# Performance work log

Hardware: AMD Instinct MI355X
Metric: run time of the kernel (lower is better)

The kernel has to match this reference:

```python
import jax, jax.numpy as jnp
import numpy as np

B, C, V, L = 64, 32, 1024, 12
ORDER = 2


def setup_inputs() -> dict:
    key = jax.random.key(0)
    ks = jax.random.split(key, 6)
    x = jax.random.normal(ks[0], (B, C, V, L), dtype=jnp.float32)
    A1 = jax.random.uniform(ks[1], (V, V), dtype=jnp.float32)
    A2 = jax.random.uniform(ks[2], (V, V), dtype=jnp.float32)
    nodevec1 = jax.random.normal(ks[3], (V, 10), dtype=jnp.float32)
    nodevec2 = jax.random.normal(ks[4], (10, V), dtype=jnp.float32)
    c_cat = (ORDER * 3 + 1) * C  # 7*C = 224, matches gcn: (order*support_len+1)*c_in
    W_mlp = jax.random.normal(ks[5], (C, c_cat), dtype=jnp.float32) * 0.05
    b_mlp = jnp.zeros((C,), dtype=jnp.float32)
    return {"x": x, "A1": A1, "A2": A2, "nodevec1": nodevec1,
            "nodevec2": nodevec2, "W_mlp": W_mlp, "b_mlp": b_mlp}


def reference(x, A1, A2, nodevec1, nodevec2, W_mlp, b_mlp):
    # adaptive adjacency: softmax(relu(E1 @ E2), dim=1)  (graph-wavenet style)
    adp = jax.nn.softmax(jax.nn.relu(nodevec1 @ nodevec2), axis=1)  # [V, V]
    supports = (A1, A2, adp)
    # gcn.forward: multi-hop diffusion via nconv einsum, order=2
    out = [x]
    for a in supports:
        x1 = jnp.einsum('ncvl,vw->ncwl', x, a)   # hop 1
        out.append(x1)
        x2 = jnp.einsum('ncvl,vw->ncwl', x1, a)  # hop 2
        out.append(x2)
    h = jnp.concatenate(out, axis=1)             # [B, 7C, V, L]
    # linear: 1x1 Conv2d over channel dim (dropout is identity in eval)
    h = jnp.einsum('ncvl,oc->novl', h, W_mlp) + b_mlp[None, :, None, None]
    return h
```

## Files before the change

### kernel.cpp

```cpp
#include <hip/hip_runtime.h>
#include <hip/hip_bf16.h>


typedef __attribute__((ext_vector_type(8))) short short8;
typedef __attribute__((ext_vector_type(4))) float floatx4;

#define V_DIM 1024
#define L_DIM 12
#define B_DIM 64
#define C_DIM 32

__global__ __launch_bounds__(128) void adp_kernel(
    const float* __restrict__ nv1, const float* __restrict__ nv2,
    float* __restrict__ adp) {
  const int v = blockIdx.x, tid = threadIdx.x;
  float n1[10];
#pragma unroll
  for (int i = 0; i < 10; ++i) n1[i] = nv1[v * 10 + i];
  __shared__ float red[128];
  float e[8];
  float lmax = -1e30f;
#pragma unroll
  for (int j = 0; j < 8; ++j) {
    int w = tid + j * 128;
    float s = 0.f;
#pragma unroll
    for (int i = 0; i < 10; ++i) s += n1[i] * nv2[i * V_DIM + w];
    s = fmaxf(s, 0.f);
    e[j] = s;
    lmax = fmaxf(lmax, s);
  }
  red[tid] = lmax; __syncthreads();
  for (int s = 64; s > 0; s >>= 1) {
    if (tid < s) red[tid] = fmaxf(red[tid], red[tid + s]);
    __syncthreads();
  }
  float mx = red[0]; __syncthreads();
  float lsum = 0.f;
#pragma unroll
  for (int j = 0; j < 8; ++j) { e[j] = __expf(e[j] - mx); lsum += e[j]; }
  red[tid] = lsum; __syncthreads();
  for (int s = 64; s > 0; s >>= 1) {
    if (tid < s) red[tid] += red[tid + s];
    __syncthreads();
  }
  float inv = 1.f / red[0];
#pragma unroll
  for (int j = 0; j < 8; ++j) adp[(size_t)v * V_DIM + tid + j * 128] = e[j] * inv;
}

__global__ __launch_bounds__(256) void cast_transpose(
    const float* __restrict__ A1, const float* __restrict__ A2,
    const float* __restrict__ adp, __hip_bfloat16* __restrict__ As,
    __hip_bfloat16* __restrict__ BtCat) {
  const int z = blockIdx.z;
  const float* src = (z == 0) ? A1 : (z == 1) ? A2 : adp;
  __hip_bfloat16* sdst = As + (size_t)z * V_DIM * V_DIM;
  __hip_bfloat16* tdst = BtCat + (size_t)(2 * z) * V_DIM * V_DIM;
  __shared__ float tile[64][65];
  const int v0 = blockIdx.y * 64, w0 = blockIdx.x * 64;
  const int tc = threadIdx.x & 15, tr = threadIdx.x >> 4;
#pragma unroll
  for (int i = 0; i < 4; ++i) {
    int r = tr + i * 16;
    float4 val = *(const float4*)(src + (size_t)(v0 + r) * V_DIM + w0 + tc * 4);
    tile[r][tc * 4 + 0] = val.x; tile[r][tc * 4 + 1] = val.y;
    tile[r][tc * 4 + 2] = val.z; tile[r][tc * 4 + 3] = val.w;
    __hip_bfloat16* sp = sdst + (size_t)(v0 + r) * V_DIM + w0 + tc * 4;
    sp[0] = __float2bfloat16(val.x); sp[1] = __float2bfloat16(val.y);
    sp[2] = __float2bfloat16(val.z); sp[3] = __float2bfloat16(val.w);
  }
  __syncthreads();
#pragma unroll
  for (int i = 0; i < 4; ++i) {
    int r = tr + i * 16;
    __hip_bfloat16* tp = tdst + (size_t)(w0 + r) * V_DIM + v0 + tc * 4;
#pragma unroll
    for (int j = 0; j < 4; ++j) tp[j] = __float2bfloat16(tile[tc * 4 + j][r]);
  }
}

__global__ __launch_bounds__(256) void transpose_x_k(
    const float* __restrict__ x, __hip_bfloat16* __restrict__ xT) {
  const int bc = blockIdx.x;
  const int b = bc >> 5, c = bc & 31;
  __shared__ __align__(16) __hip_bfloat16 tile[V_DIM * L_DIM];
  const float4* src = (const float4*)(x + (size_t)bc * (V_DIM * L_DIM));
#pragma unroll
  for (int i = 0; i < 12; ++i) {
    int idx = threadIdx.x + i * 256;
    float4 v = src[idx];
    int e = idx * 4;
    tile[e + 0] = __float2bfloat16(v.x); tile[e + 1] = __float2bfloat16(v.y);
    tile[e + 2] = __float2bfloat16(v.z); tile[e + 3] = __float2bfloat16(v.w);
  }
  __syncthreads();
  for (int l = 0; l < L_DIM; ++l) {
    __hip_bfloat16* dst = xT + ((size_t)(b * L_DIM + l) * C_DIM + c) * V_DIM;
    for (int v = threadIdx.x; v < V_DIM; v += 256) dst[v] = tile[v * L_DIM + l];
  }
}

__device__ __forceinline__ void gll16(const __hip_bfloat16* g, __hip_bfloat16* l) {
  __builtin_amdgcn_global_load_lds(
      (const __attribute__((address_space(1))) void*)g,
      (__attribute__((address_space(3))) void*)l, 16, 0, 0);
}

template <int MODE>
__global__ __launch_bounds__(256) void gemm_bt(
    const __hip_bfloat16* __restrict__ Abase,
    const __hip_bfloat16* __restrict__ Btbase,
    __hip_bfloat16* __restrict__ Cbase, int M, int N, int K,
    long long aStride, long long bStride, long long cStride) {
  const __hip_bfloat16* A = Abase + (size_t)blockIdx.z * aStride;
  const __hip_bfloat16* Bt = Btbase + (size_t)blockIdx.z * bStride;
  __hip_bfloat16* C = Cbase + (size_t)blockIdx.z * cStride;
  __shared__ __align__(16) __hip_bfloat16 lA[128 * 64];
  __shared__ __align__(16) __hip_bfloat16 lB[128 * 64];
  const int tid = threadIdx.x;
  const int wv = tid >> 6, lane = tid & 63;
  const int wm = wv >> 1, wn = wv & 1;
  const int m0 = blockIdx.y * 128, n0 = blockIdx.x * 128;
  const int lrow = lane >> 3, lcol = lane & 7;
  const int gcol = lcol ^ (lrow & 7);
  const int fr = lane & 15, quad = lane >> 4;
  const int sw = fr & 7;

  floatx4 acc[4][4];
#pragma unroll
  for (int i = 0; i < 4; ++i)
#pragma unroll
    for (int j = 0; j < 4; ++j) acc[i][j] = (floatx4){0.f, 0.f, 0.f, 0.f};

  for (int kt = 0; kt < K; kt += 64) {
    __syncthreads();
#pragma unroll
    for (int i = 0; i < 4; ++i) {
      int r0 = (wv * 4 + i) * 8;
      gll16(A + (size_t)(m0 + r0 + lrow) * K + kt + gcol * 8, &lA[r0 * 64]);
      gll16(Bt + (size_t)(n0 + r0 + lrow) * K + kt + gcol * 8, &lB[r0 * 64]);
    }
    __syncthreads();
#pragma unroll
    for (int ks = 0; ks < 2; ++ks) {
      const int chunk = (ks * 4 + quad) ^ sw;
      short8 af[4], bfr[4];
#pragma unroll
      for (int t = 0; t < 4; ++t) {
        af[t] = *(const short8*)&lA[(wm * 64 + t * 16 + fr) * 64 + chunk * 8];
        bfr[t] = *(const short8*)&lB[(wn * 64 + t * 16 + fr) * 64 + chunk * 8];
      }
#pragma unroll
      for (int i = 0; i < 4; ++i)
#pragma unroll
        for (int j = 0; j < 4; ++j)
          acc[i][j] = __builtin_amdgcn_mfma_f32_16x16x32_bf16(af[i], bfr[j], acc[i][j], 0, 0, 0);
    }
  }
#pragma unroll
  for (int i = 0; i < 4; ++i) {
#pragma unroll
    for (int j = 0; j < 4; ++j) {
      int mb = m0 + wm * 64 + i * 16 + quad * 4;
      int n = n0 + wn * 64 + j * 16 + fr;
#pragma unroll
      for (int r = 0; r < 4; ++r) {
        int m = mb + r;
        float val = acc[i][j][r];
        size_t idx;
        if (MODE == 0) {
          idx = (size_t)m * N + n;
        } else {
          int c = m & 31, bl = m >> 5, k = n >> 10, w = n & 1023;
          idx = (((size_t)bl * 6 + k) * 32 + c) * 1024 + w;
        }
        C[idx] = __float2bfloat16(val);
      }
    }
  }
}

__global__ __launch_bounds__(256) void mix_kernel(
    const __hip_bfloat16* __restrict__ R, const __hip_bfloat16* __restrict__ xT,
    const float* __restrict__ W, const float* __restrict__ bias,
    float* __restrict__ out) {
  const int b = blockIdx.y, wt = blockIdx.x;
  const int tid = threadIdx.x;
  __shared__ __align__(16) __hip_bfloat16 tile[L_DIM * C_DIM * 64];
  __shared__ float Wl[7 * 32 * 32];
  for (int i = tid; i < 7168; i += 256) {
    int o = i / 224, cc = i - o * 224;
    Wl[cc * 32 + o] = W[i];
  }
  float acc[3][32];
#pragma unroll
  for (int pt = 0; pt < 3; ++pt)
#pragma unroll
    for (int o = 0; o < 32; ++o) acc[pt][o] = bias[o];
  int wloc[3], ll[3];
#pragma unroll
  for (int pt = 0; pt < 3; ++pt) {
    int wl = tid + pt * 256;
    wloc[pt] = wl / 12;
    ll[pt] = wl - wloc[pt] * 12;
  }
  const int w0 = wt * 64;
  for (int k = 0; k < 7; ++k) {
    __syncthreads();
    const __hip_bfloat16* srcp = (k < 6) ? R : xT;
    const int rps = (k < 6) ? 192 : 32;
    const int ko = (k < 6) ? k * 32 : 0;
#pragma unroll
    for (int i = 0; i < 24; ++i) {
      int q = tid + i * 256;
      int rr = q >> 4, ci = q & 15;
      int l = rr >> 5, c = rr & 31;
      size_t rowg = (size_t)(b * L_DIM + l) * rps + ko + c;
      *(ushort4*)&tile[rr * 64 + ci * 4] =
          *(const ushort4*)&srcp[rowg * V_DIM + w0 + ci * 4];
    }
    __syncthreads();
    const float* Wp = &Wl[((k < 6) ? (k + 1) : 0) * 1024];
    const int base0 = ll[0] * 2048 + wloc[0];
    const int base1 = ll[1] * 2048 + wloc[1];
    const int base2 = ll[2] * 2048 + wloc[2];
#pragma unroll 8
    for (int c = 0; c < 32; ++c) {
      float v0 = __bfloat162float(tile[base0 + c * 64]);
      float v1 = __bfloat162float(tile[base1 + c * 64]);
      float v2 = __bfloat162float(tile[base2 + c * 64]);
#pragma unroll
      for (int o = 0; o < 32; ++o) {
        float wv = Wp[c * 32 + o];
        acc[0][o] += wv * v0;
        acc[1][o] += wv * v1;
        acc[2][o] += wv * v2;
      }
    }
  }
  const size_t obase = (size_t)b * (32 * V_DIM * L_DIM) + (size_t)w0 * L_DIM;
#pragma unroll
  for (int o = 0; o < 32; ++o) {
    size_t base = obase + (size_t)o * (V_DIM * L_DIM);
    out[base + tid] = acc[0][o];
    out[base + tid + 256] = acc[1][o];
    out[base + tid + 512] = acc[2][o];
  }
}

extern "C" void kernel_launch(void* const* d_in, const int* in_sizes, int n_in,
                              void* d_out, int out_size, void* d_ws,
                              size_t ws_size, hipStream_t stream) {
  const float* x = (const float*)d_in[0];
  const float* A1 = (const float*)d_in[1];
  const float* A2 = (const float*)d_in[2];
  const float* nv1 = (const float*)d_in[3];
  const float* nv2 = (const float*)d_in[4];
  const float* W = (const float*)d_in[5];
  const float* bias = (const float*)d_in[6];
  float* out = (float*)d_out;

  char* ws = (char*)d_ws;
  __hip_bfloat16* R = (__hip_bfloat16*)(ws + 0);
  __hip_bfloat16* xT = (__hip_bfloat16*)(ws + 301989888ull);
  __hip_bfloat16* BtCat = (__hip_bfloat16*)(ws + 352321536ull);
  __hip_bfloat16* As = (__hip_bfloat16*)(ws + 364904448ull);
  float* adp = (float*)(ws + 371195904ull);

  adp_kernel<<<dim3(1024), dim3(128), 0, stream>>>(nv1, nv2, adp);
  cast_transpose<<<dim3(16, 16, 3), dim3(256), 0, stream>>>(A1, A2, adp, As, BtCat);
  gemm_bt<0><<<dim3(8, 8, 3), dim3(256), 0, stream>>>(
      BtCat, As, BtCat + 1048576ull, 1024, 1024, 1024,
      2097152ll, 1048576ll, 2097152ll);
  transpose_x_k<<<dim3(2048), dim3(256), 0, stream>>>(x, xT);
  gemm_bt<1><<<dim3(48, 192, 1), dim3(256), 0, stream>>>(
      xT, BtCat, R, 24576, 6144, 1024, 0ll, 0ll, 0ll);
  mix_kernel<<<dim3(16, 64), dim3(256), 0, stream>>>(R, xT, W, bias, out);
}
```

Baseline: 794.5 us.

## Replace main diffusion GEMM with 256x256-tile, 4-stage pipelined MFMA kernel

Adds a dedicated GEMM kernel for the large x-by-supports product. It uses 256x256 block tiles with 512 threads and a 4-buffer LDS ring filled by direct global-to-LDS loads issued three steps ahead, with interleaved barriers and setprio around the MFMA bursts. The larger tile raises operand reuse per LDS byte, and the deep prefetch hides load latency. In exchange it uses more registers and LDS per block, which can cut occupancy, and there are fewer blocks in the grid.

```diff
diff --git a/kernel.cpp b/kernel.cpp
--- a/kernel.cpp
+++ b/kernel.cpp
@@ -181,6 +181,108 @@
   }
 }
 
+__global__ __launch_bounds__(512, 2) void gemm256(
+    const __hip_bfloat16* __restrict__ A,
+    const __hip_bfloat16* __restrict__ Bt,
+    __hip_bfloat16* __restrict__ C) {
+  constexpr int K = 1024;
+  constexpr int NH = K / 32;
+  __shared__ __align__(16) __hip_bfloat16 sA[4][8192];
+  __shared__ __align__(16) __hip_bfloat16 sB[4][8192];
+  const int tid = threadIdx.x;
+  const int wv = tid >> 6, lane = tid & 63;
+  const int wm = wv >> 2, wn = wv & 3;
+  const int fr = lane & 15, quad = lane >> 4;
+  const int rslot = (quad ^ ((fr >> 1) & 3)) << 3;
+  const int aoff = (wm * 128 + fr) * 32 + rslot;
+  const int boff = (wn * 64 + fr) * 32 + rslot;
+  const int m0 = blockIdx.y * 256, n0 = blockIdx.x * 256;
+  const int srow = wv * 32 + (lane >> 2);
+  const int gch = ((lane & 3) ^ ((lane >> 3) & 3)) << 3;
+  const __hip_bfloat16* Ag = A + (size_t)(m0 + srow) * K + gch;
+  const __hip_bfloat16* Bg = Bt + (size_t)(n0 + srow) * K + gch;
+  const int sbase = (wv * 32) * 32;
+
+  floatx4 acc[8][4];
+#pragma unroll
+  for (int i = 0; i < 8; ++i)
+#pragma unroll
+    for (int j = 0; j < 4; ++j) acc[i][j] = (floatx4){0.f, 0.f, 0.f, 0.f};
+
+#pragma unroll
+  for (int hp = 0; hp < 3; ++hp) {
+    gll16(Ag + hp * 32, &sA[hp][sbase]);
+    gll16(Ag + (size_t)16 * K + hp * 32, &sA[hp][sbase + 512]);
+    gll16(Bg + hp * 32, &sB[hp][sbase]);
+    gll16(Bg + (size_t)16 * K + hp * 32, &sB[hp][sbase + 512]);
+  }
+  asm volatile("s_waitcnt vmcnt(8)" ::: "memory");
+  __builtin_amdgcn_s_barrier();
+
+  for (int h = 0; h < NH; ++h) {
+    const int u = h & 3;
+    short8 af[4], bf[4];
+#pragma unroll
+    for (int j = 0; j < 4; ++j) bf[j] = *(const short8*)&sB[u][boff + j * 512];
+#pragma unroll
+    for (int i = 0; i < 4; ++i) af[i] = *(const short8*)&sA[u][aoff + i * 512];
+    if (h + 3 < NH) {
+      const int h3 = h + 3, u3 = h3 & 3;
+      gll16(Ag + h3 * 32, &sA[u3][sbase]);
+      gll16(Ag + (size_t)16 * K + h3 * 32, &sA[u3][sbase + 512]);
+    }
+    __builtin_amdgcn_s_barrier();
+    __builtin_amdgcn_s_setprio(1);
+#pragma unroll
+    for (int i = 0; i < 4; ++i)
+#pragma unroll
+      for (int j = 0; j < 4; ++j)
+        acc[i][j] = __builtin_amdgcn_mfma_f32_16x16x32_bf16(af[i], bf[j], acc[i][j], 0, 0, 0);
+    __builtin_amdgcn_s_setprio(0);
+    __builtin_amdgcn_s_barrier();
+#pragma unroll
+    for (int i = 0; i < 4; ++i) af[i] = *(const short8*)&sA[u][aoff + (4 + i) * 512];
+    if (h + 3 < NH) {
+      const int h3 = h + 3, u3 = h3 & 3;
+      gll16(Bg + h3 * 32, &sB[u3][sbase]);
+      gll16(Bg + (size_t)16 * K + h3 * 32, &sB[u3][sbase + 512]);
+    }
+    __builtin_amdgcn_s_barrier();
+    __builtin_amdgcn_s_setprio(1);
+#pragma unroll
+    for (int i = 0; i < 4; ++i)
+#pragma unroll
+      for (int j = 0; j < 4; ++j)
+        acc[4 + i][j] = __builtin_amdgcn_mfma_f32_16x16x32_bf16(af[i], bf[j], acc[4 + i][j], 0, 0, 0);
+    __builtin_amdgcn_s_setprio(0);
+    if (h < NH - 3) {
+      asm volatile("s_waitcnt vmcnt(8)" ::: "memory");
+    } else if (h == NH - 3) {
+      asm volatile("s_waitcnt vmcnt(4)" ::: "memory");
+    } else if (h == NH - 2) {
+      asm volatile("s_waitcnt vmcnt(0)" ::: "memory");
+    }
+    __builtin_amdgcn_s_barrier();
+  }
+
+#pragma unroll
+  for (int i = 0; i < 8; ++i) {
+#pragma unroll
+    for (int j = 0; j < 4; ++j) {
+      int mb = m0 + wm * 128 + i * 16 + quad * 4;
+      int n = n0 + wn * 64 + j * 16 + fr;
+      int k = n >> 10, w = n & 1023;
+#pragma unroll
+      for (int r = 0; r < 4; ++r) {
+        int m = mb + r;
+        int c = m & 31, bl = m >> 5;
+        size_t idx = (((size_t)bl * 6 + k) * 32 + c) * 1024 + w;
+        C[idx] = __float2bfloat16(acc[i][j][r]);
+      }
+    }
+  }
+}
+
 __global__ __launch_bounds__(256) void mix_kernel(
     const __hip_bfloat16* __restrict__ R, const __hip_bfloat16* __restrict__ xT,
     const float* __restrict__ W, const float* __restrict__ bias,
@@ -274,7 +376,6 @@
       BtCat, As, BtCat + 1048576ull, 1024, 1024, 1024,
       2097152ll, 1048576ll, 2097152ll);
   transpose_x_k<<<dim3(2048), dim3(256), 0, stream>>>(x, xT);
-  gemm_bt<1><<<dim3(48, 192, 1), dim3(256), 0, stream>>>(
-      xT, BtCat, R, 24576, 6144, 1024, 0ll, 0ll, 0ll);
+  gemm256<<<dim3(24, 96), dim3(512), 0, stream>>>(xT, BtCat, R);
   mix_kernel<<<dim3(16, 64), dim3(256), 0, stream>>>(R, xT, W, bias, out);
 }
```

Result: faster. 766.9 us (-3.5%).
